# Optimization experiments

Measured on AMD Instinct MI355X. Metric: run time of the kernel, lower is better.

Reference implementation:

```python
import jax, jax.numpy as jnp
import numpy as np

DIM = 512
BATCH, SEQ = 4, 4096


def setup_inputs() -> dict:
    key = jax.random.key(0)
    kx, kq, kk, kv, ko = jax.random.split(key, 5)
    s = DIM ** -0.5  # fan-in style init scale for stability
    return {
        "x": jax.random.normal(kx, (BATCH, SEQ, DIM), dtype=jnp.float32),
        "Wq": jax.random.normal(kq, (DIM, DIM), dtype=jnp.float32) * s,
        "Wk": jax.random.normal(kk, (DIM, DIM), dtype=jnp.float32) * s,
        "Wv": jax.random.normal(kv, (DIM, DIM), dtype=jnp.float32) * s,
        "Wo": jax.random.normal(ko, (DIM, DIM), dtype=jnp.float32) * s,
    }


def reference(x, Wq, Wk, Wv, Wo):
    # x: [B, S, D]; projections (torch Linear, no bias -> x @ W here)
    q = jnp.einsum('bsd,dk->bsk', x, Wq)  # [B,S,K]
    k = jnp.einsum('bsd,dk->bsk', x, Wk)  # [B,S,K]
    v = jnp.einsum('bsd,dv->bsv', x, Wv)  # [B,S,V]

    # sequential recurrence: M_t = M_{t-1} + v_t k_t^T ; y_t = M_t q_t
    def step(M, qkv_t):
        q_t, k_t, v_t = qkv_t  # each [B, K] / [B, V]
        M = M + v_t[:, :, None] * k_t[:, None, :]  # [B, V, K]
        y_t = jnp.einsum('bvk,bk->bv', M, q_t)
        return M, y_t

    M0 = jnp.zeros((x.shape[0], Wv.shape[1], Wk.shape[1]), dtype=x.dtype)
    qT = jnp.swapaxes(q, 0, 1)  # [S,B,K]
    kT = jnp.swapaxes(k, 0, 1)
    vT = jnp.swapaxes(v, 0, 1)
    _, ys = jax.lax.scan(step, M0, (qT, kT, vT))  # ys: [S,B,V]
    y = jnp.swapaxes(ys, 0, 1)  # [B,S,V]
    return jnp.einsum('bsv,vd->bsd', y, Wo)
```

## Files before the change

kernel.cpp:

```cpp
#include <hip/hip_runtime.h>
#include <hip/hip_bf16.h>

typedef __attribute__((ext_vector_type(8))) short bf16x8;
typedef __attribute__((ext_vector_type(4))) float f32x4;

__device__ inline short f2bf(float f) {
    __hip_bfloat16 h = __float2bfloat16(f);
    short s;
    __builtin_memcpy(&s, &h, 2);
    return s;
}
__device__ inline float bf2f(short s) {
    unsigned int u = ((unsigned int)(unsigned short)s) << 16;
    float f;
    __builtin_memcpy(&f, &u, 4);
    return f;
}

__device__ inline void cp16_async(const void* g, void* l) {
    __builtin_amdgcn_global_load_lds(
        (const __attribute__((address_space(1))) void*)g,
        (__attribute__((address_space(3))) void*)l, 16, 0, 0);
}


__global__ void prep_kernel(const float* __restrict__ x, short* __restrict__ Xb,
                            const float* __restrict__ W0, const float* __restrict__ W1,
                            const float* __restrict__ W2, const float* __restrict__ W3,
                            short* __restrict__ W4T) {
    int bid = blockIdx.x;
    if (bid < 8192) {
        int i = bid * 256 + threadIdx.x;
        float4 f = ((const float4*)x)[i];
        union { short s[4]; int2 v; } u;
        u.s[0] = f2bf(f.x); u.s[1] = f2bf(f.y); u.s[2] = f2bf(f.z); u.s[3] = f2bf(f.w);
        ((int2*)Xb)[i] = u.v;
    } else {
        int i = (bid - 8192) * 256 + threadIdx.x;
        int w = i >> 18;
        int r = i & 262143;
        int n = r >> 9, k = r & 511;
        const float* W = (w == 0) ? W0 : (w == 1) ? W1 : (w == 2) ? W2 : W3;
        W4T[i] = f2bf(W[k * 512 + n]);
    }
}


#define LDS_DECL __shared__ short sm[8][4096]

__device__ inline void stage32(const short* __restrict__ A, int lda,
                               const short* __restrict__ B, int ldb, int k0,
                               short* sA, short* sB, int tid) {
#pragma unroll
    for (int j = 0; j < 2; ++j) {
        const int L = tid * 16 + j * 4096;
        const int row = L >> 6;
        const int cb = (L & 63) ^ ((row & 3) << 4);
        cp16_async((const char*)(A + (size_t)row * lda + k0) + cb, (char*)sA + L);
        cp16_async((const char*)(B + (size_t)row * ldb + k0) + cb, (char*)sB + L);
    }
}

__device__ inline void compute32(const short* sA, const short* sB, f32x4* acc,
                                 int wr, int wc, int lr, int quad) {
    const int cb = (quad * 16) ^ ((lr & 3) << 4);
    bf16x8 af[4], bfr[4];
#pragma unroll
    for (int i = 0; i < 4; ++i)
        af[i] = *(const bf16x8*)((const char*)sA + (wr + i * 16 + lr) * 64 + cb);
#pragma unroll
    for (int j = 0; j < 4; ++j)
        bfr[j] = *(const bf16x8*)((const char*)sB + (wc + j * 16 + lr) * 64 + cb);
#pragma unroll
    for (int i = 0; i < 4; ++i)
#pragma unroll
        for (int j = 0; j < 4; ++j)
            acc[i * 4 + j] = __builtin_amdgcn_mfma_f32_16x16x32_bf16(af[i], bfr[j], acc[i * 4 + j], 0, 0, 0);
}

__device__ inline void kloop_pipe(const short* __restrict__ A, int lda,
                                  const short* __restrict__ B, int ldb, int Kd,
                                  f32x4* acc, short (*sm)[4096]) {
    const int tid = threadIdx.x, lane = tid & 63, wv = tid >> 6;
    const int quad = lane >> 4, lr = lane & 15;
    const int wr = (wv >> 1) * 64, wc = (wv & 1) * 64;
    const int NT = Kd >> 5;
    stage32(A, lda, B, ldb, 0,  sm[0], sm[1], tid);
    stage32(A, lda, B, ldb, 32, sm[2], sm[3], tid);
    stage32(A, lda, B, ldb, 64, sm[4], sm[5], tid);
    __builtin_amdgcn_sched_barrier(0);
    asm volatile("s_waitcnt vmcnt(8)" ::: "memory");
    __builtin_amdgcn_sched_barrier(0);
    __builtin_amdgcn_s_barrier();
    __builtin_amdgcn_sched_barrier(0);
    for (int t = 0; t < NT; ++t) {
        const int cur = (t & 3) << 1;
        if (t + 3 < NT)
            stage32(A, lda, B, ldb, (t + 3) << 5,
                    sm[((t + 3) & 3) << 1], sm[(((t + 3) & 3) << 1) + 1], tid);
        __builtin_amdgcn_sched_barrier(0);
        compute32(sm[cur], sm[cur + 1], acc, wr, wc, lr, quad);
        __builtin_amdgcn_sched_barrier(0);
        if (t + 3 < NT) {
            asm volatile("s_waitcnt vmcnt(8)" ::: "memory");
        } else if (t + 2 < NT) {
            asm volatile("s_waitcnt vmcnt(4)" ::: "memory");
        } else {
            asm volatile("s_waitcnt vmcnt(0)" ::: "memory");
        }
        __builtin_amdgcn_sched_barrier(0);
        __builtin_amdgcn_s_barrier();
        __builtin_amdgcn_sched_barrier(0);
    }
}

__device__ inline void store_out(float* p, float v) { *p = v; }
__device__ inline void store_out(short* p, float v) { *p = f2bf(v); }

template <typename OutT>
__device__ inline void store_tile128(OutT* C, int ldc, const f32x4* acc) {
    const int lane = threadIdx.x & 63, wv = threadIdx.x >> 6;
    const int quad = lane >> 4, lr = lane & 15;
    const int wr = (wv >> 1) * 64, wc = (wv & 1) * 64;
#pragma unroll
    for (int i = 0; i < 4; ++i)
#pragma unroll
        for (int j = 0; j < 4; ++j)
#pragma unroll
            for (int r = 0; r < 4; ++r)
                store_out(&C[(size_t)(wr + i * 16 + quad * 4 + r) * ldc + wc + j * 16 + lr],
                          acc[i * 4 + j][r]);
}

__global__ __launch_bounds__(256, 2) void proj_all(const short* __restrict__ Xb,
                                                   const short* __restrict__ W4T,
                                                   short* __restrict__ Qb, short* __restrict__ Kb,
                                                   short* __restrict__ Vt, short* __restrict__ Kt) {
    LDS_DECL;
    f32x4 acc[16];
#pragma unroll
    for (int i = 0; i < 16; ++i) acc[i] = (f32x4){0.f, 0.f, 0.f, 0.f};
    const int bid = blockIdx.x;
    const int lane = threadIdx.x & 63, wv = threadIdx.x >> 6;
    const int quad = lane >> 4, lr = lane & 15;
    const int wr = (wv >> 1) * 64, wc = (wv & 1) * 64;
    if (bid < 1024) {
        const int mt = bid >> 3, by = bid & 7;
        const short* At = Xb + (size_t)mt * 128 * 512;
        const short* Bt = W4T + (size_t)by * 128 * 512;
        short* Ct = ((by < 4) ? Qb : Kb) + (size_t)mt * 128 * 512 + (by & 3) * 128;
        kloop_pipe(At, 512, Bt, 512, 512, acc, sm);
        store_tile128(Ct, 512, acc);
        if (by >= 4) {
            const int b = mt >> 5;
            const int t0b = (mt & 31) * 128;
            const int f0 = (by - 4) * 128;
#pragma unroll
            for (int i = 0; i < 4; ++i)
#pragma unroll
                for (int j = 0; j < 4; ++j) {
                    int f = f0 + wc + j * 16 + lr;
                    int tt0 = t0b + wr + i * 16 + quad * 4;
                    short tmp[4];
#pragma unroll
                    for (int r = 0; r < 4; ++r) tmp[r] = f2bf(acc[i * 4 + j][r]);
                    *(int2*)&Kt[((size_t)b * 512 + f) * 4096 + tt0] = *(const int2*)tmp;
                }
        }
    } else {
        const int r = bid - 1024;
        const int b = r & 3, tt = (r >> 2) & 31, ft = r >> 7;
        const short* At = W4T + (size_t)2 * 262144 + (size_t)ft * 128 * 512;
        const short* Bt = Xb + ((size_t)b * 4096 + tt * 128) * 512;
        short* Ct = Vt + (size_t)b * 512 * 4096 + (size_t)ft * 128 * 4096 + tt * 128;
        kloop_pipe(At, 512, Bt, 512, 512, acc, sm);
        store_tile128(Ct, 4096, acc);
    }
}


__global__ __launch_bounds__(256, 2) void phaseA(const short* __restrict__ Vt,
                                                 const short* __restrict__ Kt,
                                                 short* __restrict__ AM) {
    LDS_DECL;
    const int bc = blockIdx.z, b = bc >> 4, c = bc & 15;
    const short* Ap = Vt + ((size_t)b * 512 + blockIdx.x * 128) * 4096 + c * 256;
    const short* Bp = Kt + ((size_t)b * 512 + blockIdx.y * 128) * 4096 + c * 256;
    short* Cp = AM + (size_t)bc * 262144 + (size_t)blockIdx.x * 128 * 512 + blockIdx.y * 128;
    f32x4 acc[16];
#pragma unroll
    for (int i = 0; i < 16; ++i) acc[i] = (f32x4){0.f, 0.f, 0.f, 0.f};
    kloop_pipe(Ap, 4096, Bp, 4096, 256, acc, sm);
    store_tile128(Cp, 512, acc);
}

__global__ __launch_bounds__(256, 2) void scan_phaseS(short* __restrict__ AM,
                                                      const short* __restrict__ Q,
                                                      const short* __restrict__ K,
                                                      short* __restrict__ P) {
    LDS_DECL;
    if (blockIdx.x < 512) {
        int i = blockIdx.x * 256 + threadIdx.x;
        int b = i >> 15;
        int vk8 = i & 32767;
        size_t base = (size_t)b * 16 * 262144 + (size_t)vk8 * 8;
        float acc[8];
#pragma unroll
        for (int s = 0; s < 8; ++s) acc[s] = 0.f;
        for (int c = 0; c < 16; ++c) {
            short* p = AM + base + (size_t)c * 262144;
            short in8[8];
            *(int4*)in8 = *(const int4*)p;
            short out8[8];
#pragma unroll
            for (int s = 0; s < 8; ++s) out8[s] = f2bf(acc[s]);
            *(int4*)p = *(const int4*)out8;
#pragma unroll
            for (int s = 0; s < 8; ++s) acc[s] += bf2f(in8[s]);
        }
        return;
    }
    const int e = blockIdx.x - 512;
    const int bc = e >> 2, mt = e & 1, nt = (e >> 1) & 1;
    if (mt < nt) return;
    const int b = bc >> 4, c = bc & 15;
    short* Pt = P + (size_t)bc * 65536 + (size_t)mt * 128 * 256 + nt * 128;
    const short* Ap = Q + ((size_t)(b * 4096 + c * 256 + mt * 128)) * 512;
    const short* Bp = K + ((size_t)(b * 4096 + c * 256 + nt * 128)) * 512;
    f32x4 acc[16];
#pragma unroll
    for (int i = 0; i < 16; ++i) acc[i] = (f32x4){0.f, 0.f, 0.f, 0.f};
    kloop_pipe(Ap, 512, Bp, 512, 512, acc, sm);
    const int lane = threadIdx.x & 63, wv = threadIdx.x >> 6;
    const int quad = lane >> 4, lr = lane & 15;
    const int wr = (wv >> 1) * 64, wc = (wv & 1) * 64;
    const bool diag = (mt == nt);
#pragma unroll
    for (int i = 0; i < 4; ++i)
#pragma unroll
        for (int j = 0; j < 4; ++j)
#pragma unroll
            for (int r = 0; r < 4; ++r) {
                int t = wr + i * 16 + quad * 4 + r;
                int jj = wc + j * 16 + lr;
                float v = (!diag || jj <= t) ? acc[i * 4 + j][r] : 0.f;
                Pt[(size_t)t * 256 + jj] = f2bf(v);
            }
}

__global__ __launch_bounds__(256, 2) void phaseY(const short* __restrict__ Q,
                                                 const short* __restrict__ Mpre,
                                                 const short* __restrict__ P,
                                                 const short* __restrict__ Vt,
                                                 short* __restrict__ Y) {
    LDS_DECL;
    const int bc = blockIdx.z, b = bc >> 4, c = bc & 15;
    const int mt = blockIdx.x, nt = blockIdx.y;
    f32x4 acc[16];
#pragma unroll
    for (int i = 0; i < 16; ++i) acc[i] = (f32x4){0.f, 0.f, 0.f, 0.f};
    const short* Ai = Q + ((size_t)(b * 4096 + c * 256 + mt * 128)) * 512;
    const short* Bi = Mpre + (size_t)bc * 262144 + (size_t)nt * 128 * 512;
    kloop_pipe(Ai, 512, Bi, 512, 512, acc, sm);
    const short* Ap = P + (size_t)bc * 65536 + (size_t)mt * 128 * 256;
    const short* Bv = Vt + ((size_t)b * 512 + nt * 128) * 4096 + c * 256;
    kloop_pipe(Ap, 256, Bv, 4096, (mt + 1) * 128, acc, sm);
    short* Cp = Y + ((size_t)(b * 4096 + c * 256 + mt * 128)) * 512 + nt * 128;
    store_tile128(Cp, 512, acc);
}

template <typename OutT>
__global__ __launch_bounds__(256, 2) void gemm128(const short* __restrict__ A, int lda,
                                                  const short* __restrict__ B, int ldb,
                                                  OutT* __restrict__ C, int ldc, int Kd) {
    LDS_DECL;
    const short* At = A + (size_t)blockIdx.x * 128 * lda;
    const short* Bt = B + (size_t)blockIdx.y * 128 * ldb;
    OutT* Ct = C + (size_t)blockIdx.x * 128 * ldc + blockIdx.y * 128;
    f32x4 acc[16];
#pragma unroll
    for (int i = 0; i < 16; ++i) acc[i] = (f32x4){0.f, 0.f, 0.f, 0.f};
    kloop_pipe(At, lda, Bt, ldb, Kd, acc, sm);
    store_tile128(Ct, ldc, acc);
}


extern "C" void kernel_launch(void* const* d_in, const int* in_sizes, int n_in,
                              void* d_out, int out_size, void* d_ws, size_t ws_size,
                              hipStream_t stream) {
    const float* x  = (const float*)d_in[0];
    const float* Wq = (const float*)d_in[1];
    const float* Wk = (const float*)d_in[2];
    const float* Wv = (const float*)d_in[3];
    const float* Wo = (const float*)d_in[4];
    float* out = (float*)d_out;

    const size_t NTD = 16384 * 512;

    short* ws  = (short*)d_ws;
    short* Xb  = ws;
    short* Qb  = Xb + NTD;
    short* Kb  = Qb + NTD;
    short* Kt  = Kb + NTD;
    short* Vt  = Kt + NTD;
    short* P   = Vt + NTD;
    short* W4T = P + 4194304;
    short* AM  = W4T + 1048576;
    short* Yb  = Kb;

    short* WoT = W4T + 3 * 262144;

    prep_kernel<<<12288, 256, 0, stream>>>(x, Xb, Wq, Wk, Wv, Wo, W4T);
    proj_all<<<1536, 256, 0, stream>>>(Xb, W4T, Qb, Kb, Vt, Kt);
    phaseA<<<dim3(4, 4, 64), 256, 0, stream>>>(Vt, Kt, AM);
    scan_phaseS<<<768, 256, 0, stream>>>(AM, Qb, Kb, P);
    phaseY<<<dim3(2, 4, 64), 256, 0, stream>>>(Qb, AM, P, Vt, Yb);
    gemm128<float><<<dim3(128, 4), 256, 0, stream>>>(Yb, 512, WoT, 512, out, 512, 512);
}
```

Before: 230.1 us.

## Fuse QKV projection into one kernel with resident X tile and pre-packed weights

Replaces the tiled proj_all GEMM with proj_qkv. Each 512-thread block loads a 128-row X tile (stored in a pre-swizzled layout) into LDS once and sweeps 768 output columns of the concatenated Wq|Wk|Wv. Weights are packed by prep_kernel directly into MFMA fragment order and read from global or L2 without LDS staging. The aim is to stop reloading X once per output tile and to cut LDS traffic and prep work. In exchange it uses 128KB of LDS per block, launches only 256 blocks, and depends on weight-fragment reads being served from cache.

```diff
diff --git a/kernel.cpp b/kernel.cpp
--- a/kernel.cpp
+++ b/kernel.cpp
@@ -23,25 +23,128 @@
         (__attribute__((address_space(3))) void*)l, 16, 0, 0);
 }
 
-
-__global__ void prep_kernel(const float* __restrict__ x, short* __restrict__ Xb,
+__global__ void prep_kernel(const float* __restrict__ x, short* __restrict__ Xp,
                             const float* __restrict__ W0, const float* __restrict__ W1,
                             const float* __restrict__ W2, const float* __restrict__ W3,
-                            short* __restrict__ W4T) {
+                            short* __restrict__ PW, short* __restrict__ WoT) {
     int bid = blockIdx.x;
-    if (bid < 8192) {
-        int i = bid * 256 + threadIdx.x;
-        float4 f = ((const float4*)x)[i];
-        union { short s[4]; int2 v; } u;
-        u.s[0] = f2bf(f.x); u.s[1] = f2bf(f.y); u.s[2] = f2bf(f.z); u.s[3] = f2bf(f.w);
-        ((int2*)Xb)[i] = u.v;
+    if (bid < 4096) {
+        int f = bid * 256 + threadIdx.x;
+        int mtf = f >> 13, r = f & 8191, kb = r >> 7, row = r & 127;
+        const float* src = x + ((size_t)(mtf * 128 + row) * 512 + kb * 8);
+        float4 a = ((const float4*)src)[0];
+        float4 bq = ((const float4*)src)[1];
+        short t[8];
+        t[0] = f2bf(a.x);  t[1] = f2bf(a.y);  t[2] = f2bf(a.z);  t[3] = f2bf(a.w);
+        t[4] = f2bf(bq.x); t[5] = f2bf(bq.y); t[6] = f2bf(bq.z); t[7] = f2bf(bq.w);
+        ((int4*)Xp)[f] = *(const int4*)t;
+    } else if (bid < 4480) {
+        int g = (bid - 4096) * 256 + threadIdx.x;
+        int lane = g & 63, ksg = (g >> 6) & 15, nn = g >> 10;
+        int w = nn >> 5;
+        int nl = (nn & 31) * 16 + (lane & 15);
+        int k0 = ksg * 32 + (lane >> 4) * 8;
+        const float* W = (w == 0) ? W0 : (w == 1) ? W1 : W2;
+        short t[8];
+#pragma unroll
+        for (int e = 0; e < 8; ++e) t[e] = f2bf(W[(size_t)(k0 + e) * 512 + nl]);
+        ((int4*)PW)[g] = *(const int4*)t;
     } else {
-        int i = (bid - 8192) * 256 + threadIdx.x;
-        int w = i >> 18;
-        int r = i & 262143;
-        int n = r >> 9, k = r & 511;
-        const float* W = (w == 0) ? W0 : (w == 1) ? W1 : (w == 2) ? W2 : W3;
-        W4T[i] = f2bf(W[k * 512 + n]);
+        int i = (bid - 4480) * 256 + threadIdx.x;
+        int n = i >> 9, k = i & 511;
+        WoT[i] = f2bf(W3[k * 512 + n]);
+    }
+}
+
+
+#define KSTEP(ks) { \
+    bf16x8 af[4], bfr[4]; \
+    _Pragma("unroll") for (int i = 0; i < 4; ++i) \
+        af[i] = *(const bf16x8*)&Xs[((ks) * 512 + quad * 128 + wm * 64 + i * 16 + lr) * 8]; \
+    _Pragma("unroll") for (int j = 0; j < 4; ++j) \
+        bfr[j] = *(const bf16x8*)&PB[((size_t)((j * 16 + (ks)) * 64 + lane)) * 8]; \
+    _Pragma("unroll") for (int i = 0; i < 4; ++i) \
+        _Pragma("unroll") for (int j = 0; j < 4; ++j) \
+            acc[i * 4 + j] = __builtin_amdgcn_mfma_f32_16x16x32_bf16(af[i], bfr[j], acc[i * 4 + j], 0, 0, 0); }
+
+__global__ __launch_bounds__(512, 2) void proj_qkv(const short* __restrict__ Xp,
+                                                   const short* __restrict__ PW,
+                                                   short* __restrict__ Qb, short* __restrict__ Kb,
+                                                   short* __restrict__ Vt, short* __restrict__ Kt) {
+    __shared__ short Xs[65536];
+    const int tid = threadIdx.x, lane = tid & 63, wv = tid >> 6;
+    const int lr = lane & 15, quad = lane >> 4;
+    const int wm = wv >> 2, wn = wv & 3;
+    const int bid = blockIdx.x;
+    const int swz = (bid & 7) * 32 + (bid >> 3);
+    const int mt = swz >> 1, half = swz & 1;
+    const short* Ap = Xp + (size_t)mt * 65536;
+#pragma unroll
+    for (int j = 0; j < 8; ++j) {
+        const int f = j * 512 + tid;
+        cp16_async(Ap + (size_t)f * 8, (char*)Xs + f * 16);
+    }
+    __builtin_amdgcn_sched_barrier(0);
+#pragma unroll
+    for (int j = 8; j < 16; ++j) {
+        const int f = j * 512 + tid;
+        cp16_async(Ap + (size_t)f * 8, (char*)Xs + f * 16);
+    }
+    __builtin_amdgcn_sched_barrier(0);
+    const int b = mt >> 5;
+    const int tl0 = (mt & 31) * 128 + wm * 64;
+    const int trow0 = mt * 128 + wm * 64;
+    for (int pass = 0; pass < 3; ++pass) {
+        const int gc0 = half * 768 + pass * 256;
+        f32x4 acc[16];
+#pragma unroll
+        for (int i = 0; i < 16; ++i) acc[i] = (f32x4){0.f, 0.f, 0.f, 0.f};
+        const short* PB = PW + (size_t)((gc0 >> 4) + wn * 4) * 8192;
+        if (pass == 0) {
+            asm volatile("s_waitcnt vmcnt(8)" ::: "memory");
+            __builtin_amdgcn_sched_barrier(0);
+            __builtin_amdgcn_s_barrier();
+            __builtin_amdgcn_sched_barrier(0);
+#pragma unroll 4
+            for (int ks = 0; ks < 8; ++ks) KSTEP(ks)
+            __builtin_amdgcn_sched_barrier(0);
+            asm volatile("s_waitcnt vmcnt(0)" ::: "memory");
+            __builtin_amdgcn_sched_barrier(0);
+            __builtin_amdgcn_s_barrier();
+            __builtin_amdgcn_sched_barrier(0);
+#pragma unroll 4
+            for (int ks = 8; ks < 16; ++ks) KSTEP(ks)
+        } else {
+#pragma unroll 4
+            for (int ks = 0; ks < 16; ++ks) KSTEP(ks)
+        }
+        const int p = gc0 >> 9;
+        const int fc0 = (gc0 & 511) + wn * 64;
+        if (p < 2) {
+            short* C = p ? Kb : Qb;
+#pragma unroll
+            for (int i = 0; i < 4; ++i)
+#pragma unroll
+                for (int j = 0; j < 4; ++j) {
+                    const size_t base = (size_t)(trow0 + i * 16 + quad * 4) * 512 + fc0 + j * 16 + lr;
+#pragma unroll
+                    for (int r = 0; r < 4; ++r)
+                        C[base + (size_t)r * 512] = f2bf(acc[i * 4 + j][r]);
+                }
+        }
+        if (p >= 1) {
+            short* T = (p == 1) ? Kt : Vt;
+#pragma unroll
+            for (int i = 0; i < 4; ++i)
+#pragma unroll
+                for (int j = 0; j < 4; ++j) {
+                    const int f = fc0 + j * 16 + lr;
+                    short tmp[4];
+#pragma unroll
+                    for (int r = 0; r < 4; ++r) tmp[r] = f2bf(acc[i * 4 + j][r]);
+                    *(int2*)&T[((size_t)b * 512 + f) * 4096 + tl0 + i * 16 + quad * 4] = *(const int2*)tmp;
+                }
+        }
     }
 }
 
@@ -132,52 +235,6 @@
                           acc[i * 4 + j][r]);
 }
 
-__global__ __launch_bounds__(256, 2) void proj_all(const short* __restrict__ Xb,
-                                                   const short* __restrict__ W4T,
-                                                   short* __restrict__ Qb, short* __restrict__ Kb,
-                                                   short* __restrict__ Vt, short* __restrict__ Kt) {
-    LDS_DECL;
-    f32x4 acc[16];
-#pragma unroll
-    for (int i = 0; i < 16; ++i) acc[i] = (f32x4){0.f, 0.f, 0.f, 0.f};
-    const int bid = blockIdx.x;
-    const int lane = threadIdx.x & 63, wv = threadIdx.x >> 6;
-    const int quad = lane >> 4, lr = lane & 15;
-    const int wr = (wv >> 1) * 64, wc = (wv & 1) * 64;
-    if (bid < 1024) {
-        const int mt = bid >> 3, by = bid & 7;
-        const short* At = Xb + (size_t)mt * 128 * 512;
-        const short* Bt = W4T + (size_t)by * 128 * 512;
-        short* Ct = ((by < 4) ? Qb : Kb) + (size_t)mt * 128 * 512 + (by & 3) * 128;
-        kloop_pipe(At, 512, Bt, 512, 512, acc, sm);
-        store_tile128(Ct, 512, acc);
-        if (by >= 4) {
-            const int b = mt >> 5;
-            const int t0b = (mt & 31) * 128;
-            const int f0 = (by - 4) * 128;
-#pragma unroll
-            for (int i = 0; i < 4; ++i)
-#pragma unroll
-                for (int j = 0; j < 4; ++j) {
-                    int f = f0 + wc + j * 16 + lr;
-                    int tt0 = t0b + wr + i * 16 + quad * 4;
-                    short tmp[4];
-#pragma unroll
-                    for (int r = 0; r < 4; ++r) tmp[r] = f2bf(acc[i * 4 + j][r]);
-                    *(int2*)&Kt[((size_t)b * 512 + f) * 4096 + tt0] = *(const int2*)tmp;
-                }
-        }
-    } else {
-        const int r = bid - 1024;
-        const int b = r & 3, tt = (r >> 2) & 31, ft = r >> 7;
-        const short* At = W4T + (size_t)2 * 262144 + (size_t)ft * 128 * 512;
-        const short* Bt = Xb + ((size_t)b * 4096 + tt * 128) * 512;
-        short* Ct = Vt + (size_t)b * 512 * 4096 + (size_t)ft * 128 * 4096 + tt * 128;
-        kloop_pipe(At, 512, Bt, 512, 512, acc, sm);
-        store_tile128(Ct, 4096, acc);
-    }
-}
-
 
 __global__ __launch_bounds__(256, 2) void phaseA(const short* __restrict__ Vt,
                                                  const short* __restrict__ Kt,
@@ -298,8 +355,8 @@
     const size_t NTD = 16384 * 512;
 
     short* ws  = (short*)d_ws;
-    short* Xb  = ws;
-    short* Qb  = Xb + NTD;
+    short* Xp  = ws;
+    short* Qb  = Xp + NTD;
     short* Kb  = Qb + NTD;
     short* Kt  = Kb + NTD;
     short* Vt  = Kt + NTD;
@@ -308,10 +365,11 @@
     short* AM  = W4T + 1048576;
     short* Yb  = Kb;
 
-    short* WoT = W4T + 3 * 262144;
-
-    prep_kernel<<<12288, 256, 0, stream>>>(x, Xb, Wq, Wk, Wv, Wo, W4T);
-    proj_all<<<1536, 256, 0, stream>>>(Xb, W4T, Qb, Kb, Vt, Kt);
+    short* PW  = W4T;
+    short* WoT = W4T + 786432;
+
+    prep_kernel<<<5504, 256, 0, stream>>>(x, Xp, Wq, Wk, Wv, Wo, PW, WoT);
+    proj_qkv<<<256, 512, 0, stream>>>(Xp, PW, Qb, Kb, Vt, Kt);
     phaseA<<<dim3(4, 4, 64), 256, 0, stream>>>(Vt, Kt, AM);
     scan_phaseS<<<768, 256, 0, stream>>>(AM, Qb, Kb, P);
     phaseY<<<dim3(2, 4, 64), 256, 0, stream>>>(Qb, AM, P, Vt, Yb);
```

New measurement: 223.7 us. -2.8%, faster.
